# Kernel optimization log

Measured on AMD Instinct MI355X. Metric: run time of the kernel, lower is better.

Reference implementation:

```python
import jax, jax.numpy as jnp
import numpy as np

CHANNELS = 64
K = 3
STRIDE = 1
GROUP_CHANNELS = 2
GROUPS = CHANNELS // GROUP_CHANNELS  # 32
RED = 4
PAD = (K - 1) // 2


def setup_inputs() -> dict:
    key = jax.random.key(0)
    ks = jax.random.split(key, 6)
    x = jax.random.normal(ks[0], (8, CHANNELS, 128, 128), dtype=jnp.float32)
    w1 = jax.random.normal(ks[1], (CHANNELS // RED, CHANNELS), dtype=jnp.float32) * 0.05
    b1 = jax.random.normal(ks[2], (CHANNELS // RED,), dtype=jnp.float32) * 0.05
    prelu_a = jnp.full((1,), 0.25, dtype=jnp.float32)
    w2 = jax.random.normal(ks[3], (K * K * GROUPS, CHANNELS // RED), dtype=jnp.float32) * 0.05
    b2 = jax.random.normal(ks[4], (K * K * GROUPS,), dtype=jnp.float32) * 0.05
    return {"x": x, "w1": w1, "b1": b1, "prelu_a": prelu_a, "w2": w2, "b2": b2}


def reference(x, w1, b1, prelu_a, w2, b2):
    # stride == 1: no avgpool
    # 1x1 conv -> PReLU -> 1x1 conv to generate per-pixel kernels
    t = jnp.einsum('bchw,oc->bohw', x, w1) + b1[None, :, None, None]
    t = jnp.where(t >= 0, t, prelu_a[0] * t)  # PReLU, single shared slope
    weight = jnp.einsum('bchw,oc->bohw', t, w2) + b2[None, :, None, None]
    b, _, h, w = weight.shape
    # (b, groups, 1, k^2, h, w)
    weight = weight.reshape(b, GROUPS, 1, K * K, h, w)
    # unfold: im2col with padding 1, stride 1; channel-major (c, kh, kw) ordering like torch.nn.Unfold
    xp = jnp.pad(x, ((0, 0), (0, 0), (PAD, PAD), (PAD, PAD)))
    patches = jnp.stack(
        [xp[:, :, i:i + h, j:j + w] for i in range(K) for j in range(K)], axis=2
    )  # (b, c, k^2, h, w)
    patches = patches.reshape(b, GROUPS, GROUP_CHANNELS, K * K, h, w)
    out = (weight * patches).sum(axis=3).reshape(b, CHANNELS, h, w)
    return out
```

## Files before the change

kernel.cpp:

```cpp
#include <hip/hip_runtime.h>

#define NPIX (128 * 128)
#define CH 64
#define RMID 16
#define KK 9
#define TOTPIX (8 * NPIX)
#define PLANE_B 65536

typedef float v2f __attribute__((ext_vector_type(2)));

__global__ __launch_bounds__(256) void conv1_kernel(
    const float* __restrict__ x,
    const float* __restrict__ w1,
    const float* __restrict__ b1,
    const float* __restrict__ prelu_a,
    float* __restrict__ t_ws)
{
    __shared__ float pl[4][64][17];

    const int c     = threadIdx.x & 63;
    const int layer = threadIdx.x >> 6;

    const int L     = blockIdx.x;
    const int bq    = L & 7;
    const int chunk = L >> 3;
    const int p     = chunk * 64 + c;
    const int G     = (bq << 14) + p;

    const float* xp = x + (size_t)bq * CH * NPIX + (size_t)(16 * layer) * NPIX + p;

    float xv[16];
#pragma unroll
    for (int k = 0; k < 16; ++k) xv[k] = xp[(size_t)k * NPIX];

    float t[RMID];
#pragma unroll
    for (int r = 0; r < RMID; ++r) t[r] = (layer == 0) ? b1[r] : 0.f;

#pragma unroll
    for (int k = 0; k < 16; ++k) {
#pragma unroll
        for (int r = 0; r < RMID; ++r)
            t[r] = fmaf(w1[r * CH + 16 * layer + k], xv[k], t[r]);
    }
#pragma unroll
    for (int r = 0; r < RMID; ++r) pl[layer][c][r] = t[r];
    __syncthreads();

    const float a  = prelu_a[0];
    const int   r0 = 4 * layer;
#pragma unroll
    for (int i = 0; i < 4; ++i) {
        float v = pl[0][c][r0 + i] + pl[1][c][r0 + i]
                + pl[2][c][r0 + i] + pl[3][c][r0 + i];
        v = (v >= 0.f) ? v : a * v;
        t_ws[(size_t)(r0 + i) * TOTPIX + G] = v;
    }
}

__global__ __launch_bounds__(256) void invol_kernel(
    const float* __restrict__ x,
    const float* __restrict__ t_ws,
    const float* __restrict__ w2,
    const float* __restrict__ b2,
    float* __restrict__ out)
{
    const int c    = threadIdx.x & 63;
    const int rsub = threadIdx.x >> 6;

    const int L     = blockIdx.x;
    const int bq    = L & 7;
    const int gq    = (L >> 3) & 7;
    const int strip = L >> 6;

    const int hq   = 4 * strip + rsub;
    const int col0 = 2 * c;
    const int p0   = hq * 128 + col0;

    const int G0 = (bq << 14) + p0;
    v2f trA[8], trB[8];
#pragma unroll
    for (int i = 0; i < 8; ++i) {
        const v2f va = *(const v2f*)(t_ws + (size_t)(2 * i)     * TOTPIX + G0);
        const v2f vb = *(const v2f*)(t_ws + (size_t)(2 * i + 1) * TOTPIX + G0);
        trA[i].x = va.x; trA[i].y = vb.x;
        trB[i].x = va.y; trB[i].y = vb.y;
    }

    const float rm0 = (hq > 0)   ? 1.f : 0.f;
    const float rm2 = (hq < 127) ? 1.f : 0.f;
    const float mL  = (c > 0)    ? 1.f : 0.f;
    const float mR  = (c < 63)   ? 1.f : 0.f;
    v2f mk[KK];
#pragma unroll
    for (int i = 0; i < 3; ++i) {
        const float rmv = (i == 0) ? rm0 : (i == 2) ? rm2 : 1.f;
        mk[i * 3 + 0].x = rmv * mL;  mk[i * 3 + 0].y = rmv;
        mk[i * 3 + 1].x = rmv;       mk[i * 3 + 1].y = rmv;
        mk[i * 3 + 2].x = rmv;       mk[i * 3 + 2].y = rmv * mR;
    }

    const int ro0 = (hq > 0)   ? -512 : 0;
    const int ro2 = (hq < 127) ?  512 : 0;

    const char* xbc = (const char*)(x   + (size_t)bq * CH * NPIX);
    char*       obc = (char*)      (out + (size_t)bq * CH * NPIX);
    const int   pb0 = 4 * p0;

#pragma unroll
    for (int gi = 0; gi < 4; ++gi) {
        const int g = 4 * gq + gi;
        const char* c0p = xbc + (size_t)(2 * g) * PLANE_B;
        const char* c1p = c0p + PLANE_B;

        const v2f a0 = *(const v2f*)(c0p + (size_t)(pb0 + ro0));
        const v2f a1 = *(const v2f*)(c0p + (size_t)pb0);
        const v2f a2 = *(const v2f*)(c0p + (size_t)(pb0 + ro2));
        const v2f e0 = *(const v2f*)(c1p + (size_t)(pb0 + ro0));
        const v2f e1 = *(const v2f*)(c1p + (size_t)pb0);
        const v2f e2 = *(const v2f*)(c1p + (size_t)(pb0 + ro2));

        v2f wgp[KK];
#pragma unroll
        for (int k = 0; k < KK; ++k) {
            const v2f* w2r2 = (const v2f*)(w2 + (g * KK + k) * RMID);
            v2f accA, accB;
            accA.x = b2[g * KK + k]; accA.y = 0.f;
            accB = accA;
#pragma unroll
            for (int r = 0; r < RMID / 2; ++r) {
                accA = __builtin_elementwise_fma(w2r2[r], trA[r], accA);
                accB = __builtin_elementwise_fma(w2r2[r], trB[r], accB);
            }
            v2f wk;
            wk.x = accA.x + accA.y;
            wk.y = accB.x + accB.y;
            wgp[k] = wk * mk[k];
        }

        const float lA0 = __shfl_up(a0.y, 1), rA0 = __shfl_down(a0.x, 1);
        const float lA1 = __shfl_up(a1.y, 1), rA1 = __shfl_down(a1.x, 1);
        const float lA2 = __shfl_up(a2.y, 1), rA2 = __shfl_down(a2.x, 1);
        const float lE0 = __shfl_up(e0.y, 1), rE0 = __shfl_down(e0.x, 1);
        const float lE1 = __shfl_up(e1.y, 1), rE1 = __shfl_down(e1.x, 1);
        const float lE2 = __shfl_up(e2.y, 1), rE2 = __shfl_down(e2.x, 1);

        v2f oA; oA.x = 0.f; oA.y = 0.f;
        v2f oB = oA;
        {
            v2f tp;
            tp.x = lA0;  tp.y = a0.x;  oA = __builtin_elementwise_fma(wgp[0], tp, oA);
                                        oA = __builtin_elementwise_fma(wgp[1], a0, oA);
            tp.x = a0.y; tp.y = rA0;   oA = __builtin_elementwise_fma(wgp[2], tp, oA);
            tp.x = lA1;  tp.y = a1.x;  oA = __builtin_elementwise_fma(wgp[3], tp, oA);
                                        oA = __builtin_elementwise_fma(wgp[4], a1, oA);
            tp.x = a1.y; tp.y = rA1;   oA = __builtin_elementwise_fma(wgp[5], tp, oA);
            tp.x = lA2;  tp.y = a2.x;  oA = __builtin_elementwise_fma(wgp[6], tp, oA);
                                        oA = __builtin_elementwise_fma(wgp[7], a2, oA);
            tp.x = a2.y; tp.y = rA2;   oA = __builtin_elementwise_fma(wgp[8], tp, oA);

            tp.x = lE0;  tp.y = e0.x;  oB = __builtin_elementwise_fma(wgp[0], tp, oB);
                                        oB = __builtin_elementwise_fma(wgp[1], e0, oB);
            tp.x = e0.y; tp.y = rE0;   oB = __builtin_elementwise_fma(wgp[2], tp, oB);
            tp.x = lE1;  tp.y = e1.x;  oB = __builtin_elementwise_fma(wgp[3], tp, oB);
                                        oB = __builtin_elementwise_fma(wgp[4], e1, oB);
            tp.x = e1.y; tp.y = rE1;   oB = __builtin_elementwise_fma(wgp[5], tp, oB);
            tp.x = lE2;  tp.y = e2.x;  oB = __builtin_elementwise_fma(wgp[6], tp, oB);
                                        oB = __builtin_elementwise_fma(wgp[7], e2, oB);
            tp.x = e2.y; tp.y = rE2;   oB = __builtin_elementwise_fma(wgp[8], tp, oB);
        }

        __builtin_nontemporal_store(oA, (v2f*)(obc + (size_t)(2 * g)     * PLANE_B + pb0));
        __builtin_nontemporal_store(oB, (v2f*)(obc + (size_t)(2 * g + 1) * PLANE_B + pb0));
    }
}

extern "C" void kernel_launch(void* const* d_in, const int* in_sizes, int n_in,
                              void* d_out, int out_size, void* d_ws, size_t ws_size,
                              hipStream_t stream)
{
    const float* x  = (const float*)d_in[0];
    const float* w1 = (const float*)d_in[1];
    const float* b1 = (const float*)d_in[2];
    const float* pa = (const float*)d_in[3];
    const float* w2 = (const float*)d_in[4];
    const float* b2 = (const float*)d_in[5];
    float* out  = (float*)d_out;
    float* t_ws = (float*)d_ws;

    hipLaunchKernelGGL(conv1_kernel, dim3(2048), dim3(256), 0, stream,
                       x, w1, b1, pa, t_ws);
    hipLaunchKernelGGL(invol_kernel, dim3(8 * 8 * 32), dim3(256), 0, stream,
                       x, t_ws, w2, b2, out);
}
```

Baseline: 127.5 us.

## Store intermediate pixel-major, vectorize conv1 over pixel pairs, halve groups per block

The conv1 kernel now handles two adjacent pixels per thread using packed v2f FMAs and writes the 16-channel intermediate in pixel-major layout (16 contiguous floats per pixel) with float4 stores. The involution kernel reads that contiguous per-pixel vector directly, and each block now covers 2 groups instead of 4, doubling the grid and issuing all x loads up front. The aim is fewer global transactions for the intermediate and more parallelism and memory-level overlap in the involution stage. In exchange, the t_ws intermediate is reloaded by twice as many blocks, and the strided per-pixel reads may coalesce less well across lanes.

```diff
diff --git a/kernel.cpp b/kernel.cpp
--- a/kernel.cpp
+++ b/kernel.cpp
@@ -16,7 +16,7 @@
     const float* __restrict__ prelu_a,
     float* __restrict__ t_ws)
 {
-    __shared__ float pl[4][64][17];
+    __shared__ v2f pl[4][64][17];
 
     const int c     = threadIdx.x & 63;
     const int layer = threadIdx.x >> 6;
@@ -24,38 +24,49 @@
     const int L     = blockIdx.x;
     const int bq    = L & 7;
     const int chunk = L >> 3;
-    const int p     = chunk * 64 + c;
-    const int G     = (bq << 14) + p;
-
-    const float* xp = x + (size_t)bq * CH * NPIX + (size_t)(16 * layer) * NPIX + p;
-
-    float xv[16];
-#pragma unroll
-    for (int k = 0; k < 16; ++k) xv[k] = xp[(size_t)k * NPIX];
-
-    float t[RMID];
-#pragma unroll
-    for (int r = 0; r < RMID; ++r) t[r] = (layer == 0) ? b1[r] : 0.f;
+    const int p0    = chunk * 128 + 2 * c;
+    const int G0    = (bq << 14) + p0;
+
+    const float* xp = x + (size_t)bq * CH * NPIX + (size_t)(16 * layer) * NPIX + p0;
+
+    v2f xv[16];
+#pragma unroll
+    for (int k = 0; k < 16; ++k) xv[k] = *(const v2f*)(xp + (size_t)k * NPIX);
+
+    v2f t2[RMID];
+#pragma unroll
+    for (int r = 0; r < RMID; ++r) {
+        const float b = (layer == 0) ? b1[r] : 0.f;
+        t2[r].x = b; t2[r].y = b;
+    }
 
 #pragma unroll
     for (int k = 0; k < 16; ++k) {
 #pragma unroll
-        for (int r = 0; r < RMID; ++r)
-            t[r] = fmaf(w1[r * CH + 16 * layer + k], xv[k], t[r]);
-    }
-#pragma unroll
-    for (int r = 0; r < RMID; ++r) pl[layer][c][r] = t[r];
+        for (int r = 0; r < RMID; ++r) {
+            const float w = w1[r * CH + 16 * layer + k];
+            v2f wv; wv.x = w; wv.y = w;
+            t2[r] = __builtin_elementwise_fma(wv, xv[k], t2[r]);
+        }
+    }
+#pragma unroll
+    for (int r = 0; r < RMID; ++r) pl[layer][c][r] = t2[r];
     __syncthreads();
 
     const float a  = prelu_a[0];
     const int   r0 = 4 * layer;
+    float s0[4], s1[4];
 #pragma unroll
     for (int i = 0; i < 4; ++i) {
-        float v = pl[0][c][r0 + i] + pl[1][c][r0 + i]
-                + pl[2][c][r0 + i] + pl[3][c][r0 + i];
-        v = (v >= 0.f) ? v : a * v;
-        t_ws[(size_t)(r0 + i) * TOTPIX + G] = v;
-    }
+        const v2f v = pl[0][c][r0 + i] + pl[1][c][r0 + i]
+                    + pl[2][c][r0 + i] + pl[3][c][r0 + i];
+        const float v0 = (v.x >= 0.f) ? v.x : a * v.x;
+        const float v1 = (v.y >= 0.f) ? v.y : a * v.y;
+        s0[i] = v0; s1[i] = v1;
+    }
+    float* tb = t_ws + (size_t)G0 * 16 + r0;
+    *(float4*)(tb)      = make_float4(s0[0], s0[1], s0[2], s0[3]);
+    *(float4*)(tb + 16) = make_float4(s1[0], s1[1], s1[2], s1[3]);
 }
 
 __global__ __launch_bounds__(256) void invol_kernel(
@@ -70,22 +81,41 @@
 
     const int L     = blockIdx.x;
     const int bq    = L & 7;
-    const int gq    = (L >> 3) & 7;
-    const int strip = L >> 6;
-
-    const int hq   = 4 * strip + rsub;
-    const int col0 = 2 * c;
-    const int p0   = hq * 128 + col0;
-
-    const int G0 = (bq << 14) + p0;
+    const int gp    = (L >> 3) & 15;
+    const int strip = L >> 7;
+
+    const int hq  = 4 * strip + rsub;
+    const int p0  = hq * 128 + 2 * c;
+    const int G0  = (bq << 14) + p0;
+    const int pb0 = 4 * p0;
+
+    const int g0 = 2 * gp, g1 = 2 * gp + 1;
+
+    const v2f* tb = (const v2f*)(t_ws + (size_t)G0 * 16);
     v2f trA[8], trB[8];
 #pragma unroll
-    for (int i = 0; i < 8; ++i) {
-        const v2f va = *(const v2f*)(t_ws + (size_t)(2 * i)     * TOTPIX + G0);
-        const v2f vb = *(const v2f*)(t_ws + (size_t)(2 * i + 1) * TOTPIX + G0);
-        trA[i].x = va.x; trA[i].y = vb.x;
-        trB[i].x = va.y; trB[i].y = vb.y;
-    }
+    for (int i = 0; i < 8; ++i) { trA[i] = tb[i]; trB[i] = tb[8 + i]; }
+
+    const int ro0 = (hq > 0)   ? -512 : 0;
+    const int ro2 = (hq < 127) ?  512 : 0;
+    const char* xbc  = (const char*)(x + (size_t)bq * CH * NPIX);
+    const char* cp00 = xbc + (size_t)(2 * g0) * PLANE_B;
+    const char* cp01 = cp00 + PLANE_B;
+    const char* cp10 = xbc + (size_t)(2 * g1) * PLANE_B;
+    const char* cp11 = cp10 + PLANE_B;
+
+    const v2f a0 = *(const v2f*)(cp00 + (size_t)(pb0 + ro0));
+    const v2f a1 = *(const v2f*)(cp00 + (size_t)pb0);
+    const v2f a2 = *(const v2f*)(cp00 + (size_t)(pb0 + ro2));
+    const v2f e0 = *(const v2f*)(cp01 + (size_t)(pb0 + ro0));
+    const v2f e1 = *(const v2f*)(cp01 + (size_t)pb0);
+    const v2f e2 = *(const v2f*)(cp01 + (size_t)(pb0 + ro2));
+    const v2f f0 = *(const v2f*)(cp10 + (size_t)(pb0 + ro0));
+    const v2f f1 = *(const v2f*)(cp10 + (size_t)pb0);
+    const v2f f2 = *(const v2f*)(cp10 + (size_t)(pb0 + ro2));
+    const v2f h0 = *(const v2f*)(cp11 + (size_t)(pb0 + ro0));
+    const v2f h1 = *(const v2f*)(cp11 + (size_t)pb0);
+    const v2f h2 = *(const v2f*)(cp11 + (size_t)(pb0 + ro2));
 
     const float rm0 = (hq > 0)   ? 1.f : 0.f;
     const float rm2 = (hq < 127) ? 1.f : 0.f;
@@ -100,25 +130,13 @@
         mk[i * 3 + 2].x = rmv;       mk[i * 3 + 2].y = rmv * mR;
     }
 
-    const int ro0 = (hq > 0)   ? -512 : 0;
-    const int ro2 = (hq < 127) ?  512 : 0;
-
-    const char* xbc = (const char*)(x   + (size_t)bq * CH * NPIX);
-    char*       obc = (char*)      (out + (size_t)bq * CH * NPIX);
-    const int   pb0 = 4 * p0;
-
-#pragma unroll
-    for (int gi = 0; gi < 4; ++gi) {
-        const int g = 4 * gq + gi;
-        const char* c0p = xbc + (size_t)(2 * g) * PLANE_B;
-        const char* c1p = c0p + PLANE_B;
-
-        const v2f a0 = *(const v2f*)(c0p + (size_t)(pb0 + ro0));
-        const v2f a1 = *(const v2f*)(c0p + (size_t)pb0);
-        const v2f a2 = *(const v2f*)(c0p + (size_t)(pb0 + ro2));
-        const v2f e0 = *(const v2f*)(c1p + (size_t)(pb0 + ro0));
-        const v2f e1 = *(const v2f*)(c1p + (size_t)pb0);
-        const v2f e2 = *(const v2f*)(c1p + (size_t)(pb0 + ro2));
+    char* obc = (char*)(out + (size_t)bq * CH * NPIX);
+
+#pragma unroll
+    for (int gi = 0; gi < 2; ++gi) {
+        const int g = (gi == 0) ? g0 : g1;
+        const v2f A0 = gi ? f0 : a0, A1 = gi ? f1 : a1, A2 = gi ? f2 : a2;
+        const v2f E0 = gi ? h0 : e0, E1 = gi ? h1 : e1, E2 = gi ? h2 : e2;
 
         v2f wgp[KK];
 #pragma unroll
@@ -138,37 +156,35 @@
             wgp[k] = wk * mk[k];
         }
 
-        const float lA0 = __shfl_up(a0.y, 1), rA0 = __shfl_down(a0.x, 1);
-        const float lA1 = __shfl_up(a1.y, 1), rA1 = __shfl_down(a1.x, 1);
-        const float lA2 = __shfl_up(a2.y, 1), rA2 = __shfl_down(a2.x, 1);
-        const float lE0 = __shfl_up(e0.y, 1), rE0 = __shfl_down(e0.x, 1);
-        const float lE1 = __shfl_up(e1.y, 1), rE1 = __shfl_down(e1.x, 1);
-        const float lE2 = __shfl_up(e2.y, 1), rE2 = __shfl_down(e2.x, 1);
+        const float lA0 = __shfl_up(A0.y, 1), rA0 = __shfl_down(A0.x, 1);
+        const float lA1 = __shfl_up(A1.y, 1), rA1 = __shfl_down(A1.x, 1);
+        const float lA2 = __shfl_up(A2.y, 1), rA2 = __shfl_down(A2.x, 1);
+        const float lE0 = __shfl_up(E0.y, 1), rE0 = __shfl_down(E0.x, 1);
+        const float lE1 = __shfl_up(E1.y, 1), rE1 = __shfl_down(E1.x, 1);
+        const float lE2 = __shfl_up(E2.y, 1), rE2 = __shfl_down(E2.x, 1);
 
         v2f oA; oA.x = 0.f; oA.y = 0.f;
         v2f oB = oA;
-        {
-            v2f tp;
-            tp.x = lA0;  tp.y = a0.x;  oA = __builtin_elementwise_fma(wgp[0], tp, oA);
-                                        oA = __builtin_elementwise_fma(wgp[1], a0, oA);
-            tp.x = a0.y; tp.y = rA0;   oA = __builtin_elementwise_fma(wgp[2], tp, oA);
-            tp.x = lA1;  tp.y = a1.x;  oA = __builtin_elementwise_fma(wgp[3], tp, oA);
-                                        oA = __builtin_elementwise_fma(wgp[4], a1, oA);
-            tp.x = a1.y; tp.y = rA1;   oA = __builtin_elementwise_fma(wgp[5], tp, oA);
-            tp.x = lA2;  tp.y = a2.x;  oA = __builtin_elementwise_fma(wgp[6], tp, oA);
-                                        oA = __builtin_elementwise_fma(wgp[7], a2, oA);
-            tp.x = a2.y; tp.y = rA2;   oA = __builtin_elementwise_fma(wgp[8], tp, oA);
-
-            tp.x = lE0;  tp.y = e0.x;  oB = __builtin_elementwise_fma(wgp[0], tp, oB);
-                                        oB = __builtin_elementwise_fma(wgp[1], e0, oB);
-            tp.x = e0.y; tp.y = rE0;   oB = __builtin_elementwise_fma(wgp[2], tp, oB);
-            tp.x = lE1;  tp.y = e1.x;  oB = __builtin_elementwise_fma(wgp[3], tp, oB);
-                                        oB = __builtin_elementwise_fma(wgp[4], e1, oB);
-            tp.x = e1.y; tp.y = rE1;   oB = __builtin_elementwise_fma(wgp[5], tp, oB);
-            tp.x = lE2;  tp.y = e2.x;  oB = __builtin_elementwise_fma(wgp[6], tp, oB);
-                                        oB = __builtin_elementwise_fma(wgp[7], e2, oB);
-            tp.x = e2.y; tp.y = rE2;   oB = __builtin_elementwise_fma(wgp[8], tp, oB);
-        }
+        v2f tp;
+        tp.x = lA0;  tp.y = A0.x;  oA = __builtin_elementwise_fma(wgp[0], tp, oA);
+                                    oA = __builtin_elementwise_fma(wgp[1], A0, oA);
+        tp.x = A0.y; tp.y = rA0;   oA = __builtin_elementwise_fma(wgp[2], tp, oA);
+        tp.x = lA1;  tp.y = A1.x;  oA = __builtin_elementwise_fma(wgp[3], tp, oA);
+                                    oA = __builtin_elementwise_fma(wgp[4], A1, oA);
+        tp.x = A1.y; tp.y = rA1;   oA = __builtin_elementwise_fma(wgp[5], tp, oA);
+        tp.x = lA2;  tp.y = A2.x;  oA = __builtin_elementwise_fma(wgp[6], tp, oA);
+                                    oA = __builtin_elementwise_fma(wgp[7], A2, oA);
+        tp.x = A2.y; tp.y = rA2;   oA = __builtin_elementwise_fma(wgp[8], tp, oA);
+
+        tp.x = lE0;  tp.y = E0.x;  oB = __builtin_elementwise_fma(wgp[0], tp, oB);
+                                    oB = __builtin_elementwise_fma(wgp[1], E0, oB);
+        tp.x = E0.y; tp.y = rE0;   oB = __builtin_elementwise_fma(wgp[2], tp, oB);
+        tp.x = lE1;  tp.y = E1.x;  oB = __builtin_elementwise_fma(wgp[3], tp, oB);
+                                    oB = __builtin_elementwise_fma(wgp[4], E1, oB);
+        tp.x = E1.y; tp.y = rE1;   oB = __builtin_elementwise_fma(wgp[5], tp, oB);
+        tp.x = lE2;  tp.y = E2.x;  oB = __builtin_elementwise_fma(wgp[6], tp, oB);
+                                    oB = __builtin_elementwise_fma(wgp[7], E2, oB);
+        tp.x = E2.y; tp.y = rE2;   oB = __builtin_elementwise_fma(wgp[8], tp, oB);
 
         __builtin_nontemporal_store(oA, (v2f*)(obc + (size_t)(2 * g)     * PLANE_B + pb0));
         __builtin_nontemporal_store(oB, (v2f*)(obc + (size_t)(2 * g + 1) * PLANE_B + pb0));
@@ -188,8 +204,8 @@
     float* out  = (float*)d_out;
     float* t_ws = (float*)d_ws;
 
-    hipLaunchKernelGGL(conv1_kernel, dim3(2048), dim3(256), 0, stream,
+    hipLaunchKernelGGL(conv1_kernel, dim3(1024), dim3(256), 0, stream,
                        x, w1, b1, pa, t_ws);
-    hipLaunchKernelGGL(invol_kernel, dim3(8 * 8 * 32), dim3(256), 0, stream,
+    hipLaunchKernelGGL(invol_kernel, dim3(4096), dim3(256), 0, stream,
                        x, t_ws, w2, b2, out);
 }
```

New measurement: 123.8 us. -2.8%, faster.
